# Optimization experiments

Hardware: AMD Instinct MI355X
Metric: run time of the kernel (lower is better)

## Reference

```python
import math
import jax, jax.numpy as jnp
import numpy as np

N = 50000
C = 128      # in_channels == out_channels
H = 8        # nhead
D = C // H   # head_dim = 16
E = 800000


def _layernorm(x, g, b, eps=1e-5):
    mu = jnp.mean(x, axis=-1, keepdims=True)
    var = jnp.var(x, axis=-1, keepdims=True)
    return (x - mu) * jax.lax.rsqrt(var + eps) * g + b


def setup_inputs() -> dict:
    key = jax.random.key(0)
    ks = jax.random.split(key, 12)
    s = 1.0 / math.sqrt(C)          # ~xavier scale
    s4 = 1.0 / math.sqrt(4 * C)
    return {
        "x": jax.random.normal(ks[0], (N, C), dtype=jnp.float32),
        "edge_index": jax.random.randint(ks[1], (2, E), 0, N, dtype=jnp.int64),
        "Wq": jax.random.normal(ks[2], (C, C), dtype=jnp.float32) * s,
        "Wk": jax.random.normal(ks[3], (C, C), dtype=jnp.float32) * s,
        "Wv": jax.random.normal(ks[4], (C, C), dtype=jnp.float32) * s,
        "Wo": jax.random.normal(ks[5], (C, C), dtype=jnp.float32) * s,
        "bo": jnp.zeros((C,), dtype=jnp.float32),
        "Wf1": jax.random.normal(ks[6], (C, 4 * C), dtype=jnp.float32) * s,
        "bf1": jnp.zeros((4 * C,), dtype=jnp.float32),
        "Wf2": jax.random.normal(ks[7], (4 * C, C), dtype=jnp.float32) * s4,
        "bf2": jnp.zeros((C,), dtype=jnp.float32),
        "g1": jnp.ones((C,), dtype=jnp.float32),
        "b1": jnp.zeros((C,), dtype=jnp.float32),
        "g2": jnp.ones((C,), dtype=jnp.float32),
        "b2": jnp.zeros((C,), dtype=jnp.float32),
    }


def reference(x, edge_index, Wq, Wk, Wv, Wo, bo, Wf1, bf1, Wf2, bf2, g1, b1, g2, b2):
    n = x.shape[0]
    loops = jnp.arange(n, dtype=edge_index.dtype)
    row = jnp.concatenate([edge_index[0], loops])  # source nodes
    col = jnp.concatenate([edge_index[1], loops])  # destination nodes

    q = (x @ Wq).reshape(n, H, D)
    k = (x @ Wk).reshape(n, H, D)
    v = (x @ Wv).reshape(n, H, D)

    # edge-level attention scores [E+N, H]
    scores = jnp.einsum('ehd,ehd->eh', q[row], k[col]) / math.sqrt(D)
    smax = jax.ops.segment_max(scores, col, num_segments=n)  # every node has a self-loop
    exp = jnp.exp(scores - smax[col])
    ssum = jax.ops.segment_sum(exp, col, num_segments=n)
    alpha = exp / (ssum[col] + 1e-8)

    out = jax.ops.segment_sum(v[row] * alpha[..., None], col, num_segments=n)
    attn = out.reshape(n, C) @ Wo + bo

    residual = x  # input_proj is Identity (in_channels == out_channels)
    x1 = _layernorm(residual + attn, g1, b1)
    ffn = jax.nn.gelu(x1 @ Wf1 + bf1, approximate=False) @ Wf2 + bf2
    return _layernorm(x1 + ffn, g2, b2)
```

## Files before the change

### kernel.cpp

```cpp
#include <hip/hip_runtime.h>
#include <cmath>


typedef short bf16x8 __attribute__((ext_vector_type(8)));
typedef float f32x4 __attribute__((ext_vector_type(4)));
typedef unsigned int uint_as1 __attribute__((address_space(1)));
typedef unsigned int uint_as3 __attribute__((address_space(3)));

__device__ inline unsigned short f2bf(float f) {
    unsigned int u = __float_as_uint(f);
    u += 0x7fffu + ((u >> 16) & 1u);
    return (unsigned short)(u >> 16);
}
__device__ inline float bflo(unsigned int w) { return __uint_as_float(w << 16); }
__device__ inline float bfhi(unsigned int w) { return __uint_as_float(w & 0xffff0000u); }

__device__ inline void gload16(const unsigned short* g, unsigned short* l) {
    __builtin_amdgcn_global_load_lds((const uint_as1*)g, (uint_as3*)l, 16, 0, 0);
}

__device__ inline float gelu_f(float x) {
    float ax = fabsf(x) * 0.70710678118f;
    float t = __builtin_amdgcn_rcpf(fmaf(0.3275911f, ax, 1.0f));
    float p = fmaf(1.061405429f, t, -1.453152027f);
    p = fmaf(p, t, 1.421413741f);
    p = fmaf(p, t, -0.284496736f);
    p = fmaf(p, t, 0.254829592f);
    p = p * t;
    float e = __expf(-ax * ax);
    float pe = p * e;
    float w = (x >= 0.f) ? (2.0f - pe) : pe;
    return 0.5f * x * w;
}


__device__ __forceinline__ void stage_panel(unsigned short* Bs,
                                            const unsigned short* base,
                                            int strideK) {
    int tid = threadIdx.x;
    int srow = tid >> 4, cc = tid & 15;
    int gc = (cc & ~7) | ((cc & 7) ^ (srow & 7));
    const unsigned short* src = base + (size_t)srow * strideK + gc * 8;
    unsigned short* dst = Bs + srow * 128 + cc * 8;
#pragma unroll
    for (int j = 0; j < 8; ++j)
        gload16(src + (size_t)j * 16 * strideK, dst + j * 16 * 128);
}

__device__ __forceinline__ void loadA_k(bf16x8 (&af)[4][4],
                                        const unsigned short* A, int M, int K,
                                        int m0, int ko, int wr, int l16, int quad) {
#pragma unroll
    for (int ti = 0; ti < 4; ++ti) {
        int row = m0 + wr * 64 + ti * 16 + l16;
        if (row > M - 1) row = M - 1;
        const unsigned short* ar = A + (size_t)row * K + ko + quad * 8;
#pragma unroll
        for (int j = 0; j < 4; ++j) af[ti][j] = *(const bf16x8*)(ar + j * 32);
    }
}

__device__ __forceinline__ void mm16(f32x4 (&acc)[4][4], const bf16x8 (&af)[4][4],
                                     const unsigned short* Bs,
                                     int wc, int quad, int l16) {
#pragma unroll
    for (int ks = 0; ks < 4; ++ks) {
        bf16x8 bfr[4];
#pragma unroll
        for (int tj = 0; tj < 4; ++tj) {
            int nr = wc * 64 + tj * 16 + l16;
            int cidx = ks * 4 + quad;
            int slot = (cidx & ~7) | ((cidx & 7) ^ (nr & 7));
            bfr[tj] = *(const bf16x8*)&Bs[nr * 128 + slot * 8];
        }
#pragma unroll
        for (int ti = 0; ti < 4; ++ti)
#pragma unroll
            for (int tj = 0; tj < 4; ++tj)
                acc[ti][tj] = __builtin_amdgcn_mfma_f32_16x16x32_bf16(
                    af[ti][ks], bfr[tj], acc[ti][tj], 0, 0, 0);
    }
}


__global__ __launch_bounds__(256) void k_init(
    const float* __restrict__ x, unsigned short* __restrict__ xb,
    const float* __restrict__ Wq, const float* __restrict__ Wk,
    const float* __restrict__ Wv, const float* __restrict__ Wo,
    const float* __restrict__ Wf1, const float* __restrict__ Wf2,
    unsigned short* __restrict__ Wqkvt, unsigned short* __restrict__ Wot,
    unsigned short* __restrict__ Wf1t, unsigned short* __restrict__ Wf2t,
    int* __restrict__ cursor, int4* __restrict__ csrz,
    int N, int nCsr4, int nCast) {
    int bid = blockIdx.x;
    int t = threadIdx.x;

    int NBc = (N + 255) >> 8;
    if (bid < NBc) {
        int i = bid * 256 + t;
        if (i < N) cursor[i] = 0;
        return;
    }
    bid -= NBc;
    int NBz = (nCsr4 + 255) >> 8;
    if (bid < NBz) {
        int i = bid * 256 + t;
        if (i < nCsr4) csrz[i] = make_int4(0, 0, 0, 0);
        return;
    }
    bid -= NBz;
    if (bid < nCast) {
        int i = bid * 256 + t;
        if (i < N * 32) {
            float4 v = ((const float4*)x)[i];
            ushort4 o;
            o.x = f2bf(v.x); o.y = f2bf(v.y); o.z = f2bf(v.z); o.w = f2bf(v.w);
            ((ushort4*)xb)[i] = o;
        }
        return;
    }
    bid -= nCast;
    int z, idx;
    if (bid < 256) { z = bid >> 6; idx = (bid & 63) * 256 + t; }
    else           { z = 4 + ((bid - 256) >> 8); idx = ((bid - 256) & 255) * 256 + t; }

    const float* in; unsigned short* out; int K, Co;
    switch (z) {
        case 0: in = Wq;  out = Wqkvt; K = 128; Co = 128; break;
        case 1: in = Wk;  out = Wqkvt; K = 128; Co = 128; break;
        case 2: in = Wv;  out = Wqkvt; K = 128; Co = 128; break;
        case 3: in = Wo;  out = Wot;   K = 128; Co = 128; break;
        case 4: in = Wf1; out = Wf1t;  K = 128; Co = 512; break;
        default: in = Wf2; out = Wf2t; K = 512; Co = 128; break;
    }
    if (idx >= K * Co) return;
    int k = idx / Co, c = idx % Co;
    int row;
    switch (z) {
        case 0: row = ((c >> 1) << 2) | (c & 1); break;
        case 1: row = 256 + c; break;
        case 2: row = (((c >> 1) << 2) | (c & 1)) + 2; break;
        default: row = c; break;
    }
    out[(size_t)row * K + k] = f2bf(in[idx]);
}


__global__ void k_fill(const int* __restrict__ ei, int* __restrict__ cursor,
                       unsigned short* __restrict__ csr, int E, int N) {
    int e = blockIdx.x * 256 + threadIdx.x;
    if (e >= E + N) return;
    int row, col;
    if (e < E) { row = ei[e]; col = ei[E + e]; }
    else       { row = col = e - E; }
    int pos = atomicAdd(&cursor[col], 1);
    csr[(size_t)col * 64 + pos] = (unsigned short)row;
}


template <int EPI, int KT>
__global__ __launch_bounds__(256) void k_gemm(
    const unsigned short* __restrict__ A, const unsigned short* __restrict__ Bt,
    const float* __restrict__ bias, const float* __restrict__ resid,
    const float* __restrict__ g, const float* __restrict__ b,
    float* __restrict__ outf, unsigned short* __restrict__ outb,
    int M, int Cout) {
    constexpr int K = KT * 128;
    __shared__ unsigned short smem[128 * 136];
    __shared__ float pS[2][128], pQ[2][128];
    float* LsF = (float*)smem;

    int tid = threadIdx.x;
    int wid = tid >> 6, lane = tid & 63;
    int quad = lane >> 4, l16 = lane & 15;
    int wr = wid >> 1, wc = wid & 1;
    int m0 = blockIdx.x * 128;
    int n0 = blockIdx.y * 128;

    f32x4 acc[4][4];
#pragma unroll
    for (int i = 0; i < 4; ++i)
#pragma unroll
        for (int j = 0; j < 4; ++j) acc[i][j] = {0.f, 0.f, 0.f, 0.f};

#pragma unroll
    for (int kt = 0; kt < KT; ++kt) {
        bf16x8 af[4][4];
        loadA_k(af, A, M, K, m0, kt * 128, wr, l16, quad);
        stage_panel(smem, Bt + (size_t)n0 * K + kt * 128, K);
        __syncthreads();
        mm16(acc, af, smem, wc, quad, l16);
        __syncthreads();
    }

    if constexpr (EPI != 2) {
        float bi[4];
        if constexpr (EPI == 1) {
#pragma unroll
            for (int tj = 0; tj < 4; ++tj) bi[tj] = bias[n0 + wc * 64 + tj * 16 + l16];
        }
#pragma unroll
        for (int ti = 0; ti < 4; ++ti)
#pragma unroll
            for (int tj = 0; tj < 4; ++tj) {
                int c = wc * 64 + tj * 16 + l16;
#pragma unroll
                for (int r = 0; r < 4; ++r) {
                    int rl = wr * 64 + ti * 16 + quad * 4 + r;
                    float v = acc[ti][tj][r];
                    if constexpr (EPI == 1) v = gelu_f(v + bi[tj]);
                    smem[rl * 136 + c] = f2bf(v);
                }
            }
        __syncthreads();
        int ch = tid & 15;
#pragma unroll
        for (int s = 0; s < 8; ++s) {
            int rl = s * 16 + (tid >> 4);
            int grow = m0 + rl;
            if (grow < M) {
                uint4 v = *(const uint4*)&smem[rl * 136 + ch * 8];
                *(uint4*)&outb[(size_t)grow * Cout + n0 + ch * 8] = v;
            }
        }
    } else {
        float bi[4], gv[4], bv[4];
#pragma unroll
        for (int tj = 0; tj < 4; ++tj) {
            int col = wc * 64 + tj * 16 + l16;
            bi[tj] = bias[col]; gv[tj] = g[col]; bv[tj] = b[col];
        }
#pragma unroll
        for (int ti = 0; ti < 4; ++ti)
#pragma unroll
            for (int tj = 0; tj < 4; ++tj) {
                int col = wc * 64 + tj * 16 + l16;
#pragma unroll
                for (int r = 0; r < 4; ++r) {
                    int row = m0 + wr * 64 + ti * 16 + quad * 4 + r;
                    float rv = (row < M) ? resid[(size_t)row * 128 + col] : 0.f;
                    acc[ti][tj][r] += bi[tj] + rv;
                }
            }
#pragma unroll
        for (int ti = 0; ti < 4; ++ti)
#pragma unroll
            for (int r = 0; r < 4; ++r) {
                float s = acc[ti][0][r] + acc[ti][1][r] + acc[ti][2][r] + acc[ti][3][r];
                float q = acc[ti][0][r] * acc[ti][0][r] + acc[ti][1][r] * acc[ti][1][r]
                        + acc[ti][2][r] * acc[ti][2][r] + acc[ti][3][r] * acc[ti][3][r];
                s += __shfl_xor(s, 1); q += __shfl_xor(q, 1);
                s += __shfl_xor(s, 2); q += __shfl_xor(q, 2);
                s += __shfl_xor(s, 4); q += __shfl_xor(q, 4);
                s += __shfl_xor(s, 8); q += __shfl_xor(q, 8);
                if (l16 == 0) {
                    int lr = wr * 64 + ti * 16 + quad * 4 + r;
                    pS[wc][lr] = s; pQ[wc][lr] = q;
                }
            }
        __syncthreads();
        if (tid < 128) {
            float s = pS[0][tid] + pS[1][tid];
            float q = pQ[0][tid] + pQ[1][tid];
            float mean = s * 0.0078125f;
            float var = q * 0.0078125f - mean * mean;
            pS[0][tid] = mean;
            pQ[0][tid] = rsqrtf(var + 1e-5f);
        }
        __syncthreads();

        if (outb) {
#pragma unroll
            for (int ti = 0; ti < 4; ++ti)
#pragma unroll
                for (int r = 0; r < 4; ++r) {
                    int lr = wr * 64 + ti * 16 + quad * 4 + r;
                    float mean = pS[0][lr], rs = pQ[0][lr];
#pragma unroll
                    for (int tj = 0; tj < 4; ++tj) {
                        int col = wc * 64 + tj * 16 + l16;
                        smem[lr * 136 + col] =
                            f2bf((acc[ti][tj][r] - mean) * rs * gv[tj] + bv[tj]);
                    }
                }
            __syncthreads();
            int ch = tid & 15;
#pragma unroll
            for (int s = 0; s < 8; ++s) {
                int rl = s * 16 + (tid >> 4);
                int grow = m0 + rl;
                if (grow < M) {
                    uint4 v = *(const uint4*)&smem[rl * 136 + ch * 8];
                    *(uint4*)&outb[(size_t)grow * 128 + ch * 8] = v;
                }
            }
        }
        if (outf) {
#pragma unroll
            for (int p = 0; p < 2; ++p) {
                __syncthreads();
                if (wr == p) {
#pragma unroll
                    for (int ti = 0; ti < 4; ++ti)
#pragma unroll
                        for (int r = 0; r < 4; ++r) {
                            int lr = wr * 64 + ti * 16 + quad * 4 + r;
                            float mean = pS[0][lr], rs = pQ[0][lr];
#pragma unroll
                            for (int tj = 0; tj < 4; ++tj) {
                                int col = wc * 64 + tj * 16 + l16;
                                LsF[(lr - p * 64) * 128 + col] =
                                    (acc[ti][tj][r] - mean) * rs * gv[tj] + bv[tj];
                            }
                        }
                }
                __syncthreads();
                int ch = tid & 31;
#pragma unroll
                for (int s = 0; s < 8; ++s) {
                    int rl = s * 8 + (tid >> 5);
                    int grow = m0 + p * 64 + rl;
                    if (grow < M) {
                        float4 v = *(const float4*)&LsF[rl * 128 + ch * 4];
                        *(float4*)&outf[(size_t)grow * 128 + ch * 4] = v;
                    }
                }
            }
        }
    }
}


__global__ __launch_bounds__(256) void k_attn(
    const unsigned int* __restrict__ qkv, const int* __restrict__ counts,
    const unsigned short* __restrict__ csr, unsigned int* __restrict__ ob,
    int N) {
    int j = blockIdx.x * 4 + (threadIdx.x >> 6);
    if (j >= N) return;
    int l = threadIdx.x & 63;
    int lk = l & 31;
    int half = l >> 5;
    const uint4* qv4 = (const uint4*)qkv;

    uint2 kw = *(const uint2*)(qkv + (size_t)j * 192 + 128 + lk * 2);
    const float S = 0.36067376022224085f;
    float k0 = bflo(kw.x) * S, k1 = bfhi(kw.x) * S;
    float k2 = bflo(kw.y) * S, k3 = bfhi(kw.y) * S;

    int cnt = counts[j];
    int nb = (cnt + 3) >> 2;
    const unsigned short* cp = csr + (size_t)j * 64;

    int ra0 = cp[half],     rb0 = cp[2 + half];
    int ra1 = cp[4 + half], rb1 = cp[6 + half];
    uint4 gA = qv4[(unsigned)ra0 * 48u + lk];
    uint4 gB = qv4[(unsigned)rb0 * 48u + lk];

    float lsum = 0.f, a0 = 0.f, a1 = 0.f, a2 = 0.f, a3 = 0.f;
    for (int bi = 0; bi < nb; ++bi) {
        int ra2 = cp[(bi + 2) * 4 + half];
        int rb2 = cp[(bi + 2) * 4 + 2 + half];
        uint4 nA = qv4[(unsigned)ra1 * 48u + lk];
        uint4 nB = qv4[(unsigned)rb1 * 48u + lk];

        int rem = cnt - bi * 4;
        {
            float s = fmaf(bflo(gA.x), k0,
                      fmaf(bfhi(gA.x), k1,
                      fmaf(bflo(gA.z), k2, bfhi(gA.z) * k3)));
            s += __shfl_xor(s, 1);
            s += __shfl_xor(s, 2);
            float e = exp2f(s);
            e = (half < rem) ? e : 0.f;
            lsum += e;
            a0 = fmaf(e, bflo(gA.y), a0); a1 = fmaf(e, bfhi(gA.y), a1);
            a2 = fmaf(e, bflo(gA.w), a2); a3 = fmaf(e, bfhi(gA.w), a3);
        }
        {
            float s = fmaf(bflo(gB.x), k0,
                      fmaf(bfhi(gB.x), k1,
                      fmaf(bflo(gB.z), k2, bfhi(gB.z) * k3)));
            s += __shfl_xor(s, 1);
            s += __shfl_xor(s, 2);
            float e = exp2f(s);
            e = (2 + half < rem) ? e : 0.f;
            lsum += e;
            a0 = fmaf(e, bflo(gB.y), a0); a1 = fmaf(e, bfhi(gB.y), a1);
            a2 = fmaf(e, bflo(gB.w), a2); a3 = fmaf(e, bfhi(gB.w), a3);
        }
        gA = nA; gB = nB; ra1 = ra2; rb1 = rb2;
    }

    lsum += __shfl_xor(lsum, 32);
    a0 += __shfl_xor(a0, 32); a1 += __shfl_xor(a1, 32);
    a2 += __shfl_xor(a2, 32); a3 += __shfl_xor(a3, 32);

    if (half == 0) {
        float inv = 1.f / (lsum + 1e-8f);
        uint2 o;
        o.x = ((unsigned int)f2bf(a1 * inv) << 16) | (unsigned int)f2bf(a0 * inv);
        o.y = ((unsigned int)f2bf(a3 * inv) << 16) | (unsigned int)f2bf(a2 * inv);
        *(uint2*)(ob + (size_t)j * 64 + lk * 2) = o;
    }
}


extern "C" void kernel_launch(void* const* d_in, const int* in_sizes, int n_in,
                              void* d_out, int out_size, void* d_ws, size_t ws_size,
                              hipStream_t stream) {
    const float* x   = (const float*)d_in[0];
    const int* ei    = (const int*)d_in[1];
    const float* Wq  = (const float*)d_in[2];
    const float* Wk  = (const float*)d_in[3];
    const float* Wv  = (const float*)d_in[4];
    const float* Wo  = (const float*)d_in[5];
    const float* bo  = (const float*)d_in[6];
    const float* Wf1 = (const float*)d_in[7];
    const float* bf1 = (const float*)d_in[8];
    const float* Wf2 = (const float*)d_in[9];
    const float* bf2 = (const float*)d_in[10];
    const float* g1  = (const float*)d_in[11];
    const float* b1  = (const float*)d_in[12];
    const float* g2  = (const float*)d_in[13];
    const float* b2  = (const float*)d_in[14];

    int N = in_sizes[0] / 128;
    int E = in_sizes[1] / 2;
    int N2 = ((N + 127) / 128) * 128;
    int NE = E + N;

    char* p = (char*)d_ws;
    auto alloc = [&](size_t bytes) -> char* {
        char* r = p;
        p += (bytes + 255) & ~(size_t)255;
        return r;
    };
    unsigned short* qkv = (unsigned short*)alloc((size_t)N2 * 512 * 2);
    unsigned short* ob  = qkv + (size_t)N2 * 384;
    unsigned short* hb  = qkv;
    unsigned short* x1b = (unsigned short*)alloc((size_t)N2 * 128 * 2);
    unsigned short* xb  = x1b;
    float* x1f          = (float*)alloc((size_t)N2 * 128 * 4);
    unsigned short* Wqkvt = (unsigned short*)alloc(384 * 128 * 2);
    unsigned short* Wot   = (unsigned short*)alloc(128 * 128 * 2);
    unsigned short* Wf1t  = (unsigned short*)alloc(512 * 128 * 2);
    unsigned short* Wf2t  = (unsigned short*)alloc(128 * 512 * 2);
    int* cursor = (int*)alloc((size_t)N * 4);
    unsigned short* csr = (unsigned short*)alloc(((size_t)N * 64 + 256) * 2);

    int nCsr4 = N * 8 + 32;
    int nCast = (N * 32 + 255) / 256;
    int nInit = ((N + 255) / 256) + ((nCsr4 + 255) / 256) + nCast + 768;
    int M128 = (N + 127) / 128;

    k_init<<<nInit, 256, 0, stream>>>(x, xb, Wq, Wk, Wv, Wo, Wf1, Wf2,
                                      Wqkvt, Wot, Wf1t, Wf2t,
                                      cursor, (int4*)csr, N, nCsr4, nCast);
    k_fill<<<(NE + 255) / 256, 256, 0, stream>>>(ei, cursor, csr, E, N);

    k_gemm<0, 1><<<dim3(M128, 3), 256, 0, stream>>>(
        xb, Wqkvt, nullptr, nullptr, nullptr, nullptr, nullptr, qkv, N, 384);

    k_attn<<<(N + 3) / 4, 256, 0, stream>>>((const unsigned int*)qkv, cursor,
                                            csr, (unsigned int*)ob, N);

    k_gemm<2, 1><<<dim3(M128, 1), 256, 0, stream>>>(
        ob, Wot, bo, x, g1, b1, x1f, x1b, N, 128);

    k_gemm<1, 1><<<dim3(M128, 4), 256, 0, stream>>>(
        x1b, Wf1t, bf1, nullptr, nullptr, nullptr, nullptr, hb, N, 512);

    k_gemm<2, 4><<<dim3(M128, 1), 256, 0, stream>>>(
        hb, Wf2t, bf2, x1f, g2, b2, (float*)d_out, nullptr, N, 128);
}
```

Baseline: 320.9 us.

## Split GEMM into weight-resident M-looping kernel and K-looping LayerNorm kernel

The single templated GEMM becomes two kernels. k_gemmM stages the 128x128 weight panel in LDS once and reuses it across two M tiles per block, with a flat grid that interleaves the N-panel index. k_gemmK handles the K=512 FFN down-projection with a fused LayerNorm. Both now write outputs straight from accumulators with scalar stores instead of staging them through LDS for 16-byte coalesced stores, which saves LDS traffic and barriers but risks poorly coalesced global writes.

```diff
diff --git a/kernel.cpp b/kernel.cpp
--- a/kernel.cpp
+++ b/kernel.cpp
@@ -158,24 +158,144 @@
 }
 
 
-template <int EPI, int KT>
-__global__ __launch_bounds__(256) void k_gemm(
+template <int EPI, int MT>
+__global__ __launch_bounds__(256) void k_gemmM(
     const unsigned short* __restrict__ A, const unsigned short* __restrict__ Bt,
     const float* __restrict__ bias, const float* __restrict__ resid,
     const float* __restrict__ g, const float* __restrict__ b,
     float* __restrict__ outf, unsigned short* __restrict__ outb,
-    int M, int Cout) {
+    int M, int Cout, int NZ) {
+    __shared__ unsigned short Bs[128 * 128];
+    __shared__ float pS[2][128], pQ[2][128];
+
+    int tid = threadIdx.x;
+    int wid = tid >> 6, lane = tid & 63;
+    int quad = lane >> 4, l16 = lane & 15;
+    int wr = wid >> 1, wc = wid & 1;
+    int bid = blockIdx.x;
+    int zi = bid % NZ;
+    int ci = bid / NZ;
+    int n0 = zi * 128;
+
+    stage_panel(Bs, Bt + (size_t)n0 * 128, 128);
+    __syncthreads();
+#pragma unroll
+    for (int mt = 0; mt < MT; ++mt) {
+        int m0 = (ci * MT + mt) * 128;
+        if (m0 >= M) continue;
+
+        bf16x8 af[4][4];
+        loadA_k(af, A, M, 128, m0, 0, wr, l16, quad);
+
+        f32x4 acc[4][4];
+#pragma unroll
+        for (int i = 0; i < 4; ++i)
+#pragma unroll
+            for (int j = 0; j < 4; ++j) acc[i][j] = {0.f, 0.f, 0.f, 0.f};
+        mm16(acc, af, Bs, wc, quad, l16);
+
+        if constexpr (EPI != 2) {
+            float bi[4];
+            if constexpr (EPI == 1) {
+#pragma unroll
+                for (int tj = 0; tj < 4; ++tj)
+                    bi[tj] = bias[n0 + wc * 64 + tj * 16 + l16];
+            }
+#pragma unroll
+            for (int ti = 0; ti < 4; ++ti)
+#pragma unroll
+                for (int tj = 0; tj < 4; ++tj) {
+                    int col = n0 + wc * 64 + tj * 16 + l16;
+#pragma unroll
+                    for (int r = 0; r < 4; ++r) {
+                        int row = m0 + wr * 64 + ti * 16 + quad * 4 + r;
+                        if (row >= M) continue;
+                        float v = acc[ti][tj][r];
+                        if constexpr (EPI == 1) v = gelu_f(v + bi[tj]);
+                        outb[(size_t)row * Cout + col] = f2bf(v);
+                    }
+                }
+        } else {
+            float bi[4], gv[4], bv[4];
+#pragma unroll
+            for (int tj = 0; tj < 4; ++tj) {
+                int col = wc * 64 + tj * 16 + l16;
+                bi[tj] = bias[col]; gv[tj] = g[col]; bv[tj] = b[col];
+            }
+#pragma unroll
+            for (int ti = 0; ti < 4; ++ti)
+#pragma unroll
+                for (int tj = 0; tj < 4; ++tj) {
+                    int col = wc * 64 + tj * 16 + l16;
+#pragma unroll
+                    for (int r = 0; r < 4; ++r) {
+                        int row = m0 + wr * 64 + ti * 16 + quad * 4 + r;
+                        float rv = (row < M) ? resid[(size_t)row * 128 + col] : 0.f;
+                        acc[ti][tj][r] += bi[tj] + rv;
+                    }
+                }
+#pragma unroll
+            for (int ti = 0; ti < 4; ++ti)
+#pragma unroll
+                for (int r = 0; r < 4; ++r) {
+                    float s = acc[ti][0][r] + acc[ti][1][r] + acc[ti][2][r] + acc[ti][3][r];
+                    float q = acc[ti][0][r] * acc[ti][0][r] + acc[ti][1][r] * acc[ti][1][r]
+                            + acc[ti][2][r] * acc[ti][2][r] + acc[ti][3][r] * acc[ti][3][r];
+                    s += __shfl_xor(s, 1); q += __shfl_xor(q, 1);
+                    s += __shfl_xor(s, 2); q += __shfl_xor(q, 2);
+                    s += __shfl_xor(s, 4); q += __shfl_xor(q, 4);
+                    s += __shfl_xor(s, 8); q += __shfl_xor(q, 8);
+                    if (l16 == 0) {
+                        int lr = wr * 64 + ti * 16 + quad * 4 + r;
+                        pS[wc][lr] = s; pQ[wc][lr] = q;
+                    }
+                }
+            __syncthreads();
+            if (tid < 128) {
+                float s = pS[0][tid] + pS[1][tid];
+                float q = pQ[0][tid] + pQ[1][tid];
+                float mean = s * 0.0078125f;
+                float var = q * 0.0078125f - mean * mean;
+                pS[0][tid] = mean;
+                pQ[0][tid] = rsqrtf(var + 1e-5f);
+            }
+            __syncthreads();
+#pragma unroll
+            for (int ti = 0; ti < 4; ++ti)
+#pragma unroll
+                for (int r = 0; r < 4; ++r) {
+                    int lr = wr * 64 + ti * 16 + quad * 4 + r;
+                    int row = m0 + lr;
+                    if (row >= M) continue;
+                    float mean = pS[0][lr], rs = pQ[0][lr];
+#pragma unroll
+                    for (int tj = 0; tj < 4; ++tj) {
+                        int col = wc * 64 + tj * 16 + l16;
+                        float y = (acc[ti][tj][r] - mean) * rs * gv[tj] + bv[tj];
+                        if (outf) outf[(size_t)row * 128 + col] = y;
+                        if (outb) outb[(size_t)row * 128 + col] = f2bf(y);
+                    }
+                }
+        }
+    }
+}
+
+
+template <int KT>
+__global__ __launch_bounds__(256) void k_gemmK(
+    const unsigned short* __restrict__ A, const unsigned short* __restrict__ Bt,
+    const float* __restrict__ bias, const float* __restrict__ resid,
+    const float* __restrict__ g, const float* __restrict__ b,
+    float* __restrict__ outf, int M) {
     constexpr int K = KT * 128;
-    __shared__ unsigned short smem[128 * 136];
+    __shared__ unsigned short smem[128 * 128];
     __shared__ float pS[2][128], pQ[2][128];
-    float* LsF = (float*)smem;
 
     int tid = threadIdx.x;
     int wid = tid >> 6, lane = tid & 63;
     int quad = lane >> 4, l16 = lane & 15;
     int wr = wid >> 1, wc = wid & 1;
     int m0 = blockIdx.x * 128;
-    int n0 = blockIdx.y * 128;
 
     f32x4 acc[4][4];
 #pragma unroll
@@ -187,147 +307,71 @@
     for (int kt = 0; kt < KT; ++kt) {
         bf16x8 af[4][4];
         loadA_k(af, A, M, K, m0, kt * 128, wr, l16, quad);
-        stage_panel(smem, Bt + (size_t)n0 * K + kt * 128, K);
+        stage_panel(smem, Bt + kt * 128, K);
         __syncthreads();
         mm16(acc, af, smem, wc, quad, l16);
         __syncthreads();
     }
 
-    if constexpr (EPI != 2) {
-        float bi[4];
-        if constexpr (EPI == 1) {
-#pragma unroll
-            for (int tj = 0; tj < 4; ++tj) bi[tj] = bias[n0 + wc * 64 + tj * 16 + l16];
-        }
-#pragma unroll
-        for (int ti = 0; ti < 4; ++ti)
-#pragma unroll
-            for (int tj = 0; tj < 4; ++tj) {
-                int c = wc * 64 + tj * 16 + l16;
-#pragma unroll
-                for (int r = 0; r < 4; ++r) {
-                    int rl = wr * 64 + ti * 16 + quad * 4 + r;
-                    float v = acc[ti][tj][r];
-                    if constexpr (EPI == 1) v = gelu_f(v + bi[tj]);
-                    smem[rl * 136 + c] = f2bf(v);
-                }
-            }
-        __syncthreads();
-        int ch = tid & 15;
-#pragma unroll
-        for (int s = 0; s < 8; ++s) {
-            int rl = s * 16 + (tid >> 4);
-            int grow = m0 + rl;
-            if (grow < M) {
-                uint4 v = *(const uint4*)&smem[rl * 136 + ch * 8];
-                *(uint4*)&outb[(size_t)grow * Cout + n0 + ch * 8] = v;
-            }
-        }
-    } else {
-        float bi[4], gv[4], bv[4];
+    float bi[4], gv[4], bv[4];
+#pragma unroll
+    for (int tj = 0; tj < 4; ++tj) {
+        int col = wc * 64 + tj * 16 + l16;
+        bi[tj] = bias[col]; gv[tj] = g[col]; bv[tj] = b[col];
+    }
+#pragma unroll
+    for (int ti = 0; ti < 4; ++ti)
 #pragma unroll
         for (int tj = 0; tj < 4; ++tj) {
             int col = wc * 64 + tj * 16 + l16;
-            bi[tj] = bias[col]; gv[tj] = g[col]; bv[tj] = b[col];
-        }
-#pragma unroll
-        for (int ti = 0; ti < 4; ++ti)
+#pragma unroll
+            for (int r = 0; r < 4; ++r) {
+                int row = m0 + wr * 64 + ti * 16 + quad * 4 + r;
+                float rv = (row < M) ? resid[(size_t)row * 128 + col] : 0.f;
+                acc[ti][tj][r] += bi[tj] + rv;
+            }
+        }
+#pragma unroll
+    for (int ti = 0; ti < 4; ++ti)
+#pragma unroll
+        for (int r = 0; r < 4; ++r) {
+            float s = acc[ti][0][r] + acc[ti][1][r] + acc[ti][2][r] + acc[ti][3][r];
+            float q = acc[ti][0][r] * acc[ti][0][r] + acc[ti][1][r] * acc[ti][1][r]
+                    + acc[ti][2][r] * acc[ti][2][r] + acc[ti][3][r] * acc[ti][3][r];
+            s += __shfl_xor(s, 1); q += __shfl_xor(q, 1);
+            s += __shfl_xor(s, 2); q += __shfl_xor(q, 2);
+            s += __shfl_xor(s, 4); q += __shfl_xor(q, 4);
+            s += __shfl_xor(s, 8); q += __shfl_xor(q, 8);
+            if (l16 == 0) {
+                int lr = wr * 64 + ti * 16 + quad * 4 + r;
+                pS[wc][lr] = s; pQ[wc][lr] = q;
+            }
+        }
+    __syncthreads();
+    if (tid < 128) {
+        float s = pS[0][tid] + pS[1][tid];
+        float q = pQ[0][tid] + pQ[1][tid];
+        float mean = s * 0.0078125f;
+        float var = q * 0.0078125f - mean * mean;
+        pS[0][tid] = mean;
+        pQ[0][tid] = rsqrtf(var + 1e-5f);
+    }
+    __syncthreads();
+#pragma unroll
+    for (int ti = 0; ti < 4; ++ti)
+#pragma unroll
+        for (int r = 0; r < 4; ++r) {
+            int lr = wr * 64 + ti * 16 + quad * 4 + r;
+            int row = m0 + lr;
+            if (row >= M) continue;
+            float mean = pS[0][lr], rs = pQ[0][lr];
 #pragma unroll
             for (int tj = 0; tj < 4; ++tj) {
                 int col = wc * 64 + tj * 16 + l16;
-#pragma unroll
-                for (int r = 0; r < 4; ++r) {
-                    int row = m0 + wr * 64 + ti * 16 + quad * 4 + r;
-                    float rv = (row < M) ? resid[(size_t)row * 128 + col] : 0.f;
-                    acc[ti][tj][r] += bi[tj] + rv;
-                }
+                outf[(size_t)row * 128 + col] =
+                    (acc[ti][tj][r] - mean) * rs * gv[tj] + bv[tj];
             }
-#pragma unroll
-        for (int ti = 0; ti < 4; ++ti)
-#pragma unroll
-            for (int r = 0; r < 4; ++r) {
-                float s = acc[ti][0][r] + acc[ti][1][r] + acc[ti][2][r] + acc[ti][3][r];
-                float q = acc[ti][0][r] * acc[ti][0][r] + acc[ti][1][r] * acc[ti][1][r]
-                        + acc[ti][2][r] * acc[ti][2][r] + acc[ti][3][r] * acc[ti][3][r];
-                s += __shfl_xor(s, 1); q += __shfl_xor(q, 1);
-                s += __shfl_xor(s, 2); q += __shfl_xor(q, 2);
-                s += __shfl_xor(s, 4); q += __shfl_xor(q, 4);
-                s += __shfl_xor(s, 8); q += __shfl_xor(q, 8);
-                if (l16 == 0) {
-                    int lr = wr * 64 + ti * 16 + quad * 4 + r;
-                    pS[wc][lr] = s; pQ[wc][lr] = q;
-                }
-            }
-        __syncthreads();
-        if (tid < 128) {
-            float s = pS[0][tid] + pS[1][tid];
-            float q = pQ[0][tid] + pQ[1][tid];
-            float mean = s * 0.0078125f;
-            float var = q * 0.0078125f - mean * mean;
-            pS[0][tid] = mean;
-            pQ[0][tid] = rsqrtf(var + 1e-5f);
-        }
-        __syncthreads();
-
-        if (outb) {
-#pragma unroll
-            for (int ti = 0; ti < 4; ++ti)
-#pragma unroll
-                for (int r = 0; r < 4; ++r) {
-                    int lr = wr * 64 + ti * 16 + quad * 4 + r;
-                    float mean = pS[0][lr], rs = pQ[0][lr];
-#pragma unroll
-                    for (int tj = 0; tj < 4; ++tj) {
-                        int col = wc * 64 + tj * 16 + l16;
-                        smem[lr * 136 + col] =
-                            f2bf((acc[ti][tj][r] - mean) * rs * gv[tj] + bv[tj]);
-                    }
-                }
-            __syncthreads();
-            int ch = tid & 15;
-#pragma unroll
-            for (int s = 0; s < 8; ++s) {
-                int rl = s * 16 + (tid >> 4);
-                int grow = m0 + rl;
-                if (grow < M) {
-                    uint4 v = *(const uint4*)&smem[rl * 136 + ch * 8];
-                    *(uint4*)&outb[(size_t)grow * 128 + ch * 8] = v;
-                }
-            }
-        }
-        if (outf) {
-#pragma unroll
-            for (int p = 0; p < 2; ++p) {
-                __syncthreads();
-                if (wr == p) {
-#pragma unroll
-                    for (int ti = 0; ti < 4; ++ti)
-#pragma unroll
-                        for (int r = 0; r < 4; ++r) {
-                            int lr = wr * 64 + ti * 16 + quad * 4 + r;
-                            float mean = pS[0][lr], rs = pQ[0][lr];
-#pragma unroll
-                            for (int tj = 0; tj < 4; ++tj) {
-                                int col = wc * 64 + tj * 16 + l16;
-                                LsF[(lr - p * 64) * 128 + col] =
-                                    (acc[ti][tj][r] - mean) * rs * gv[tj] + bv[tj];
-                            }
-                        }
-                }
-                __syncthreads();
-                int ch = tid & 31;
-#pragma unroll
-                for (int s = 0; s < 8; ++s) {
-                    int rl = s * 8 + (tid >> 5);
-                    int grow = m0 + p * 64 + rl;
-                    if (grow < M) {
-                        float4 v = *(const float4*)&LsF[rl * 128 + ch * 4];
-                        *(float4*)&outf[(size_t)grow * 128 + ch * 4] = v;
-                    }
-                }
-            }
-        }
-    }
+        }
 }
 
 
@@ -452,24 +496,26 @@
     int nCast = (N * 32 + 255) / 256;
     int nInit = ((N + 255) / 256) + ((nCsr4 + 255) / 256) + nCast + 768;
     int M128 = (N + 127) / 128;
+    int MC2  = (M128 + 1) / 2;
 
     k_init<<<nInit, 256, 0, stream>>>(x, xb, Wq, Wk, Wv, Wo, Wf1, Wf2,
                                       Wqkvt, Wot, Wf1t, Wf2t,
                                       cursor, (int4*)csr, N, nCsr4, nCast);
     k_fill<<<(NE + 255) / 256, 256, 0, stream>>>(ei, cursor, csr, E, N);
 
-    k_gemm<0, 1><<<dim3(M128, 3), 256, 0, stream>>>(
-        xb, Wqkvt, nullptr, nullptr, nullptr, nullptr, nullptr, qkv, N, 384);
+    k_gemmM<0, 2><<<3 * MC2, 256, 0, stream>>>(
+        xb, Wqkvt, nullptr, nullptr, nullptr, nullptr, nullptr, qkv,
+        N, 384, 3);
 
     k_attn<<<(N + 3) / 4, 256, 0, stream>>>((const unsigned int*)qkv, cursor,
                                             csr, (unsigned int*)ob, N);
 
-    k_gemm<2, 1><<<dim3(M128, 1), 256, 0, stream>>>(
-        ob, Wot, bo, x, g1, b1, x1f, x1b, N, 128);
-
-    k_gemm<1, 1><<<dim3(M128, 4), 256, 0, stream>>>(
-        x1b, Wf1t, bf1, nullptr, nullptr, nullptr, nullptr, hb, N, 512);
-
-    k_gemm<2, 4><<<dim3(M128, 1), 256, 0, stream>>>(
-        hb, Wf2t, bf2, x1f, g2, b2, (float*)d_out, nullptr, N, 128);
-}
+    k_gemmM<2, 1><<<M128, 256, 0, stream>>>(
+        ob, Wot, bo, x, g1, b1, x1f, x1b, N, 128, 1);
+
+    k_gemmM<1, 2><<<4 * MC2, 256, 0, stream>>>(
+        x1b, Wf1t, bf1, nullptr, nullptr, nullptr, nullptr, hb, N, 512, 4);
+
+    k_gemmK<4><<<M128, 256, 0, stream>>>(
+        hb, Wf2t, bf2, x1f, g2, b2, (float*)d_out, N);
+}
```

Result: slower. 349.9 us (+9.0%).
